# Kernel tuning notes

Hardware: AMD Instinct MI355X
Metric: run time of the kernel (lower is better)

## Reference

```python
import jax, jax.numpy as jnp
import numpy as np

COEF = 0.97


def setup_inputs() -> dict:
    key = jax.random.key(0)
    B, C, T = 32, 1, 262144
    x = jax.random.normal(key, (B, C, T), dtype=jnp.float32)
    return {"input": x}


def reference(input) -> jnp.ndarray:
    # input: (B, 1, T). torch RNN(1,1,bias=False) with w_ih=1, w_hh=coef and
    # default tanh nonlinearity computes h[t] = tanh(x[t] + coef * h[t-1]), h[-1]=0.
    x = input[:, 0, :]                      # (B, T)
    xt = jnp.swapaxes(x, 0, 1)              # (T, B) for scan over time

    def step(h, x_t):
        h = jnp.tanh(x_t + COEF * h)
        return h, h

    h0 = jnp.zeros(x.shape[0], dtype=x.dtype)
    _, ys = jax.lax.scan(step, h0, xt)      # ys: (T, B)
    return jnp.swapaxes(ys, 0, 1)[:, None, :]  # (B, 1, T)
```

## Files before the change

kernel.cpp:

```cpp
#include <hip/hip_runtime.h>


#define T_LEN 262144
#define WSTR  36
#define NROWS 66

__device__ __forceinline__ float vexp2f(float x) {
#if __has_builtin(__builtin_amdgcn_exp2f)
    return __builtin_amdgcn_exp2f(x);
#else
    float r; asm("v_exp_f32 %0, %1" : "=v"(r) : "v"(x)); return r;
#endif
}
__device__ __forceinline__ float vrcpf(float x) {
#if __has_builtin(__builtin_amdgcn_rcpf)
    return __builtin_amdgcn_rcpf(x);
#else
    float r; asm("v_rcp_f32 %0, %1" : "=v"(r) : "v"(x)); return r;
#endif
}

__device__ __forceinline__ float step(float r, float b) {
    const float A = -2.0f * 2.8853900817779268f * 0.97f;
    return vrcpf(vexp2f(fmaf(A, r, b)) + 1.0f);
}

__global__ __launch_bounds__(64) void ipe_kernel(const float* __restrict__ x,
                                                 float* __restrict__ out) {
    __shared__ float lds[NROWS * WSTR];

    const float K  = 2.8853900817779268f;
    const float Kc = K * 0.97f;

    const int lane = threadIdx.x;
    const int row  = blockIdx.x >> 7;
    const int wb   = blockIdx.x & 127;

    const float4* __restrict__ xr =
        reinterpret_cast<const float4*>(x) + (size_t)row * (T_LEN / 4);

    #pragma unroll
    for (int m = 0; m < 8; ++m) {
        int g4 = (wb << 9) - 8 + (m << 6) + lane;
        int g4c = (m == 0 && g4 < 0) ? 0 : g4;
        float4 v = xr[g4c];
        if (m == 0 && g4 < 0) v = make_float4(0.f, 0.f, 0.f, 0.f);
        int w4 = (m << 6) + lane;
        int dw = (w4 >> 3) * WSTR + ((w4 & 7) << 2);
        *reinterpret_cast<float4*>(&lds[dw]) = v;
    }
    if (lane < 8) {
        int g4 = (wb << 9) + 504 + lane;
        float4 v = xr[g4];
        int dw = 64 * WSTR + (lane << 2);
        *reinterpret_cast<float4*>(&lds[dw]) = v;
    }
    __syncthreads();

    int addr = lane * WSTR;
    float4 cur = *reinterpret_cast<const float4*>(&lds[addr]);
    float r = 0.5f;

    #pragma unroll
    for (int jj = 0; jj < 8; ++jj) {
        int naddr = addr + ((jj == 7) ? 8 : 4);
        float4 nxt = *reinterpret_cast<const float4*>(&lds[naddr]);
        float b0 = fmaf(K, cur.x, Kc);
        float b1 = fmaf(K, cur.y, Kc);
        float b2 = fmaf(K, cur.z, Kc);
        float b3 = fmaf(K, cur.w, Kc);
        r = step(r, b0);
        r = step(r, b1);
        r = step(r, b2);
        r = step(r, b3);
        addr = naddr; cur = nxt;
    }

    #pragma unroll
    for (int jj = 0; jj < 8; ++jj) {
        int naddr = addr + ((jj == 7) ? 8 : 4);
        float4 nxt = *reinterpret_cast<const float4*>(&lds[naddr]);
        float b0 = fmaf(K, cur.x, Kc);
        float b1 = fmaf(K, cur.y, Kc);
        float b2 = fmaf(K, cur.z, Kc);
        float b3 = fmaf(K, cur.w, Kc);
        float4 o;
        r = step(r, b0); o.x = fmaf(-2.0f, r, 1.0f);
        r = step(r, b1); o.y = fmaf(-2.0f, r, 1.0f);
        r = step(r, b2); o.z = fmaf(-2.0f, r, 1.0f);
        r = step(r, b3); o.w = fmaf(-2.0f, r, 1.0f);
        *reinterpret_cast<float4*>(&lds[addr]) = o;
        addr = naddr; cur = nxt;
    }
    __syncthreads();

    float4* __restrict__ ov = reinterpret_cast<float4*>(out)
        + (size_t)row * (T_LEN / 4) + (size_t)wb * 512;
    #pragma unroll
    for (int m = 0; m < 8; ++m) {
        int o4 = (m << 6) + lane;
        int dw = ((o4 >> 3) + 1) * WSTR + ((o4 & 7) << 2);
        float4 v = *reinterpret_cast<const float4*>(&lds[dw]);
        ov[o4] = v;
    }
}

extern "C" void kernel_launch(void* const* d_in, const int* in_sizes, int n_in,
                              void* d_out, int out_size, void* d_ws, size_t ws_size,
                              hipStream_t stream) {
    const float* x = (const float*)d_in[0];
    float* out = (float*)d_out;

    int B = in_sizes[0] / T_LEN;
    int blocks = B * 128;
    ipe_kernel<<<blocks, 64, 0, stream>>>(x, out);
}
```

Baseline: 16.64 us.

## Halve per-lane chunk to 16 outputs and pack four wavefronts per block

Each lane now produces 16 outputs after a 32-step warm-up instead of 32 outputs, which halves the serial dependent chain in the output phase. Work per wave drops to 1024 elements, so twice as many waves cover the sequence. Four waves are grouped into a 256-thread block, each with its own padded LDS slice. The warm-up stays at 32 steps, so the redundant warm-up work grows relative to useful output. Adding the lane<16 tail load and clamping it keeps the halo correct at the end of a row.

```diff
diff --git a/kernel.cpp b/kernel.cpp
--- a/kernel.cpp
+++ b/kernel.cpp
@@ -2,8 +2,7 @@
 
 
 #define T_LEN 262144
-#define WSTR  36
-#define NROWS 66
+#define WLDS  1224
 
 __device__ __forceinline__ float vexp2f(float x) {
 #if __has_builtin(__builtin_amdgcn_exp2f)
@@ -25,46 +24,55 @@
     return vrcpf(vexp2f(fmaf(A, r, b)) + 1.0f);
 }
 
-__global__ __launch_bounds__(64) void ipe_kernel(const float* __restrict__ x,
-                                                 float* __restrict__ out) {
-    __shared__ float lds[NROWS * WSTR];
+__global__ __launch_bounds__(256, 8) void ipe_kernel(const float* __restrict__ x,
+                                                     float* __restrict__ out) {
+    __shared__ float lds[4 * WLDS];
 
     const float K  = 2.8853900817779268f;
     const float Kc = K * 0.97f;
 
-    const int lane = threadIdx.x;
-    const int row  = blockIdx.x >> 7;
-    const int wb   = blockIdx.x & 127;
+    const int lane = threadIdx.x & 63;
+    const int wiw  = threadIdx.x >> 6;
+    const int gw   = blockIdx.x * 4 + wiw;
+    const int row  = gw >> 8;
+    const int wb   = gw & 255;
 
+    float* __restrict__ w = &lds[wiw * WLDS];
     const float4* __restrict__ xr =
         reinterpret_cast<const float4*>(x) + (size_t)row * (T_LEN / 4);
 
     #pragma unroll
-    for (int m = 0; m < 8; ++m) {
-        int g4 = (wb << 9) - 8 + (m << 6) + lane;
-        int g4c = (m == 0 && g4 < 0) ? 0 : g4;
+    for (int m = 0; m < 4; ++m) {
+        int w4 = (m << 6) + lane;
+        int g4 = (wb << 8) - 8 + w4;
+        int g4c = (g4 < 0) ? 0 : g4;
         float4 v = xr[g4c];
-        if (m == 0 && g4 < 0) v = make_float4(0.f, 0.f, 0.f, 0.f);
-        int w4 = (m << 6) + lane;
-        int dw = (w4 >> 3) * WSTR + ((w4 & 7) << 2);
-        *reinterpret_cast<float4*>(&lds[dw]) = v;
+        if (g4 < 0) v = make_float4(0.f, 0.f, 0.f, 0.f);
+        int q = w4 << 2;
+        int dw = q + ((q >> 5) << 2);
+        *reinterpret_cast<float4*>(&w[dw]) = v;
     }
-    if (lane < 8) {
-        int g4 = (wb << 9) + 504 + lane;
+    if (lane < 16) {
+        int w4 = 256 + lane;
+        int g4 = (wb << 8) - 8 + w4;
+        if (g4 > T_LEN / 4 - 1) g4 = T_LEN / 4 - 1;
         float4 v = xr[g4];
-        int dw = 64 * WSTR + (lane << 2);
-        *reinterpret_cast<float4*>(&lds[dw]) = v;
+        int q = w4 << 2;
+        int dw = q + ((q >> 5) << 2);
+        *reinterpret_cast<float4*>(&w[dw]) = v;
     }
     __syncthreads();
 
-    int addr = lane * WSTR;
-    float4 cur = *reinterpret_cast<const float4*>(&lds[addr]);
+    int p = lane << 4;
+    int a = p + ((p >> 5) << 2);
+    float4 cur = *reinterpret_cast<const float4*>(&w[a]);
     float r = 0.5f;
 
     #pragma unroll
     for (int jj = 0; jj < 8; ++jj) {
-        int naddr = addr + ((jj == 7) ? 8 : 4);
-        float4 nxt = *reinterpret_cast<const float4*>(&lds[naddr]);
+        int pn = p + 4;
+        int an = pn + ((pn >> 5) << 2);
+        float4 nxt = *reinterpret_cast<const float4*>(&w[an]);
         float b0 = fmaf(K, cur.x, Kc);
         float b1 = fmaf(K, cur.y, Kc);
         float b2 = fmaf(K, cur.z, Kc);
@@ -73,13 +81,14 @@
         r = step(r, b1);
         r = step(r, b2);
         r = step(r, b3);
-        addr = naddr; cur = nxt;
+        p = pn; a = an; cur = nxt;
     }
 
     #pragma unroll
-    for (int jj = 0; jj < 8; ++jj) {
-        int naddr = addr + ((jj == 7) ? 8 : 4);
-        float4 nxt = *reinterpret_cast<const float4*>(&lds[naddr]);
+    for (int jj = 0; jj < 4; ++jj) {
+        int pn = p + 4;
+        int an = pn + ((pn >> 5) << 2);
+        float4 nxt = *reinterpret_cast<const float4*>(&w[an]);
         float b0 = fmaf(K, cur.x, Kc);
         float b1 = fmaf(K, cur.y, Kc);
         float b2 = fmaf(K, cur.z, Kc);
@@ -89,18 +98,19 @@
         r = step(r, b1); o.y = fmaf(-2.0f, r, 1.0f);
         r = step(r, b2); o.z = fmaf(-2.0f, r, 1.0f);
         r = step(r, b3); o.w = fmaf(-2.0f, r, 1.0f);
-        *reinterpret_cast<float4*>(&lds[addr]) = o;
-        addr = naddr; cur = nxt;
+        *reinterpret_cast<float4*>(&w[a]) = o;
+        p = pn; a = an; cur = nxt;
     }
     __syncthreads();
 
     float4* __restrict__ ov = reinterpret_cast<float4*>(out)
-        + (size_t)row * (T_LEN / 4) + (size_t)wb * 512;
+        + (size_t)row * (T_LEN / 4) + ((size_t)wb << 8);
     #pragma unroll
-    for (int m = 0; m < 8; ++m) {
+    for (int m = 0; m < 4; ++m) {
         int o4 = (m << 6) + lane;
-        int dw = ((o4 >> 3) + 1) * WSTR + ((o4 & 7) << 2);
-        float4 v = *reinterpret_cast<const float4*>(&lds[dw]);
+        int q = (o4 << 2) + 32;
+        int dw = q + ((q >> 5) << 2);
+        float4 v = *reinterpret_cast<const float4*>(&w[dw]);
         ov[o4] = v;
     }
 }
@@ -112,6 +122,6 @@
     float* out = (float*)d_out;
 
     int B = in_sizes[0] / T_LEN;
-    int blocks = B * 128;
-    ipe_kernel<<<blocks, 64, 0, stream>>>(x, out);
+    int blocks = B * 64;
+    ipe_kernel<<<blocks, 256, 0, stream>>>(x, out);
 }
```

Measured after the change: 17.93 us. +7.7%, slower.
